# Optimization experiments

Measured on AMD Instinct MI355X. Metric: run time of the kernel, lower is better.

Reference implementation:

```python
import jax, jax.numpy as jnp
import numpy as np

N = 50000       # num_nodes
R = 32          # num_relations
H = 16          # hidden channels
C = 8           # num_classes
E = 1_600_000   # num_edges (avg degree 32)


def setup_inputs() -> dict:
    key = jax.random.key(0)
    ks = jax.random.split(key, 8)
    edge_index = jax.random.randint(ks[0], (2, E), 0, N, dtype=jnp.int64)
    edge_type = jnp.sort(jax.random.randint(ks[1], (E,), 0, R, dtype=jnp.int64))
    s1 = 1.0 / np.sqrt(N)
    s2 = 1.0 / np.sqrt(H)
    return {
        "edge_index": edge_index,
        "edge_type": edge_type,
        "weight1": jax.random.normal(ks[2], (R, N, H), jnp.float32) * s1,
        "root1": jax.random.normal(ks[3], (N, H), jnp.float32) * s1,
        "bias1": jnp.zeros((H,), jnp.float32),
        "weight2": jax.random.normal(ks[4], (R, H, C), jnp.float32) * s2,
        "root2": jax.random.normal(ks[5], (H, C), jnp.float32) * s2,
        "bias2": jnp.zeros((C,), jnp.float32),
    }


def reference(edge_index, edge_type, weight1, root1, bias1, weight2, root2, bias2):
    # R-GCN with mean aggregation per relation (PyG RGCNConv semantics).
    src, dst = edge_index[0], edge_index[1]
    # combined segment id: one segment per (relation, dst node)
    seg = edge_type * N + dst  # [E]
    ones = jnp.ones((E,), weight1.dtype)
    cnt = jax.ops.segment_sum(ones, seg, num_segments=R * N)          # [R*N]
    denom = jnp.maximum(cnt, 1.0)[:, None]

    # ---- layer 1: x = None -> identity features; message_r(j) = weight1[r, j] ----
    msg1 = weight1[edge_type, src]                                     # [E, H] gather
    mean1 = jax.ops.segment_sum(msg1, seg, num_segments=R * N) / denom # [R*N, H]
    h = mean1.reshape(R, N, H).sum(0) + root1 + bias1                  # [N, H]
    h = jax.nn.relu(h)

    # ---- layer 2: aggregate features per relation, then relation-specific GEMM ----
    msg2 = h[src]                                                       # [E, H]
    mean2 = jax.ops.segment_sum(msg2, seg, num_segments=R * N) / denom  # [R*N, H]
    mean2 = mean2.reshape(R, N, H)
    out = jnp.einsum('rnf,rfo->no', mean2, weight2) + h @ root2 + bias2 # [N, C]
    return jax.nn.log_softmax(out, axis=1)
```

## Files before the change

kernel.cpp:

```cpp
#include <hip/hip_runtime.h>
#include <math.h>

#define NN 50000
#define RR 32
#define HH 16
#define CC 8
#define SHIFT 6
#define BSZ 64
#define NB 782
#define CAP 2560
#define G 256
#define BINS (BSZ * RR)
#define SCH 64

static __device__ __forceinline__ unsigned short f2bf(float x) {
    unsigned u = __float_as_uint(x);
    unsigned r = (u + 0x7FFF + ((u >> 16) & 1)) >> 16;
    return (unsigned short)r;
}


__global__ void hist_k(const int* __restrict__ dst, int* __restrict__ hist, int E) {
    __shared__ int lh[NB];
    int g = blockIdx.x, tid = threadIdx.x;
    for (int j = tid; j < NB; j += 256) lh[j] = 0;
    __syncthreads();
    int chunk = (E + G - 1) / G;
    int beg = g * chunk, end = min(beg + chunk, E);
    for (int i = beg + tid; i < end; i += 256)
        atomicAdd(&lh[dst[i] >> SHIFT], 1);
    __syncthreads();
    for (int j = tid; j < NB; j += 256) hist[g * NB + j] = lh[j];
}

__global__ void scanAC_k(const int* __restrict__ hist, int* __restrict__ pos,
                         int* __restrict__ btot) {
    __shared__ int lds[G];
    int b = blockIdx.x, t = threadIdx.x;
    int v = hist[t * NB + b];
    lds[t] = v;
    __syncthreads();
    for (int ofs = 1; ofs < G; ofs <<= 1) {
        int add = (t >= ofs) ? lds[t - ofs] : 0;
        __syncthreads();
        lds[t] += add;
        __syncthreads();
    }
    pos[t * NB + b] = b * CAP + lds[t] - v;
    if (t == G - 1) btot[b] = lds[t];
}

__global__ void scatter2_k(const int* __restrict__ src, const int* __restrict__ dst,
                           const int* __restrict__ et, const int* __restrict__ pos,
                           unsigned* __restrict__ bucket, int E) {
    __shared__ int cur[NB];
    int g = blockIdx.x, tid = threadIdx.x;
    for (int j = tid; j < NB; j += 256) cur[j] = pos[g * NB + j];
    __syncthreads();
    int chunk = (E + G - 1) / G;
    int beg = g * chunk, end = min(beg + chunk, E);
    for (int i = beg + tid; i < end; i += 256) {
        int d = dst[i];
        int p = atomicAdd(&cur[d >> SHIFT], 1);
        bucket[p] = (unsigned)src[i] | ((unsigned)et[i] << 16) |
                    ((unsigned)(d & (BSZ - 1)) << 21);
    }
}


__global__ __launch_bounds__(256) void sortfin_k(
        const unsigned* __restrict__ bucket, const int* __restrict__ btot,
        unsigned* __restrict__ sorted, int* __restrict__ off2,
        float* __restrict__ inv) {
    __shared__ int bins[BINS];
    __shared__ unsigned stage[CAP];
    __shared__ int ts[256];
    int b = blockIdx.x, t = threadIdx.x;
    int e0 = b * CAP, n = btot[b];
    int d0 = b * BSZ;
    int ndst = NN - d0; if (ndst > BSZ) ndst = BSZ;
    for (int j = t; j < BINS; j += 256) bins[j] = 0;
    __syncthreads();
    for (int i = t; i < n; i += 256) {
        unsigned rec = bucket[e0 + i];
        int key = ((rec >> 21) & 63) * RR + ((rec >> 16) & 31);
        atomicAdd(&bins[key], 1);
    }
    __syncthreads();
    for (int j = t; j < ndst * RR; j += 256)
        inv[d0 * RR + j] = 1.0f / fmaxf((float)bins[j], 1.0f);
    int loc[8]; int s = 0;
#pragma unroll
    for (int k = 0; k < 8; ++k) { loc[k] = bins[t * 8 + k]; s += loc[k]; }
    ts[t] = s;
    __syncthreads();
    for (int ofs = 1; ofs < 256; ofs <<= 1) {
        int add = (t >= ofs) ? ts[t - ofs] : 0;
        __syncthreads();
        ts[t] += add;
        __syncthreads();
    }
    int run = ts[t] - s;
    __syncthreads();
#pragma unroll
    for (int k = 0; k < 8; ++k) { int c = loc[k]; bins[t * 8 + k] = run; run += c; }
    __syncthreads();
    for (int dl = t; dl < BSZ; dl += 256) off2[b * 65 + dl] = e0 + bins[dl * RR];
    if (t == 0) off2[b * 65 + 64] = e0 + n;
    __syncthreads();
    for (int i = t; i < n; i += 256) {
        unsigned rec = bucket[e0 + i];
        int key = ((rec >> 21) & 63) * RR + ((rec >> 16) & 31);
        int p = atomicAdd(&bins[key], 1);
        stage[p] = rec & 0x1FFFFF;
    }
    __syncthreads();
    for (int i = t; i < n; i += 256) sorted[e0 + i] = stage[i];
}


__global__ __launch_bounds__(256) void layer1_k(
        const unsigned* __restrict__ sorted, const int* __restrict__ off2,
        const float* __restrict__ inv, const float4* __restrict__ w1v,
        const float4* __restrict__ root1v, const float4* __restrict__ bias1v,
        float4* __restrict__ hv) {
    int d = (blockIdx.x * blockDim.x + threadIdx.x) >> 6;
    if (d >= NN) return;
    int lane = threadIdx.x & 63;
    int q = lane & 3, eo = lane >> 2;
    int idx = (d >> 6) * 65 + (d & 63);
    int b0 = off2[idx], b1 = off2[idx + 1];
    const float* invd = inv + d * RR;

    unsigned rec[4]; float sc[4];
#pragma unroll
    for (int k = 0; k < 4; ++k) {
        int i = b0 + eo + k * 16;
        bool ok = i < b1;
        rec[k] = ok ? sorted[i] : 0u;
        sc[k]  = ok ? invd[(rec[k] >> 16) & 31] : 0.f;
    }
    float4 w[4];
#pragma unroll
    for (int k = 0; k < 4; ++k)
        w[k] = w1v[(size_t)(((rec[k] >> 16) & 31) * NN + (rec[k] & 0xFFFF)) * 4 + q];
    float ax = 0.f, ay = 0.f, az = 0.f, aw = 0.f;
#pragma unroll
    for (int k = 0; k < 4; ++k) {
        ax += w[k].x * sc[k]; ay += w[k].y * sc[k];
        az += w[k].z * sc[k]; aw += w[k].w * sc[k];
    }
    for (int i = b0 + 64 + eo; i < b1; i += 16) {
        unsigned rr = sorted[i];
        float s2 = invd[(rr >> 16) & 31];
        float4 ww = w1v[(size_t)(((rr >> 16) & 31) * NN + (rr & 0xFFFF)) * 4 + q];
        ax += ww.x * s2; ay += ww.y * s2; az += ww.z * s2; aw += ww.w * s2;
    }
#pragma unroll
    for (int m = 4; m < 64; m <<= 1) {
        ax += __shfl_xor(ax, m); ay += __shfl_xor(ay, m);
        az += __shfl_xor(az, m); aw += __shfl_xor(aw, m);
    }
    if (lane < 4) {
        float4 rt = root1v[d * 4 + lane];
        float4 bs = bias1v[lane];
        float4 o;
        o.x = fmaxf(ax + rt.x + bs.x, 0.f);
        o.y = fmaxf(ay + rt.y + bs.y, 0.f);
        o.z = fmaxf(az + rt.z + bs.z, 0.f);
        o.w = fmaxf(aw + rt.w + bs.w, 0.f);
        hv[d * 4 + lane] = o;
    }
}


__global__ __launch_bounds__(256) void hwbuild_k(
        const float* __restrict__ h, const float* __restrict__ w2,
        unsigned* __restrict__ hw2u) {
    __shared__ float4 hs[SCH * 4];
    int tid = threadIdx.x;
    int nl = tid >> 7;
    int k  = tid & 127;
    int r  = k >> 2;
    int c0 = (k & 3) * 2;
    float wa[HH], wb[HH];
    {
        const float* base = w2 + r * HH * CC;
#pragma unroll
        for (int f = 0; f < HH; ++f) {
            wa[f] = base[f * CC + c0];
            wb[f] = base[f * CC + c0 + 1];
        }
    }
    int s0 = blockIdx.x * SCH;
    int nnodes = NN - s0; if (nnodes > SCH) nnodes = SCH;
    const float4* hg = (const float4*)(h + s0 * HH);
    for (int j = tid; j < nnodes * 4; j += 256) hs[j] = hg[j];
    __syncthreads();
    for (int sl = nl; sl < nnodes; sl += 2) {
        float4 h0 = hs[sl * 4 + 0], h1 = hs[sl * 4 + 1];
        float4 h2 = hs[sl * 4 + 2], h3 = hs[sl * 4 + 3];
        float hr[HH] = {h0.x, h0.y, h0.z, h0.w, h1.x, h1.y, h1.z, h1.w,
                        h2.x, h2.y, h2.z, h2.w, h3.x, h3.y, h3.z, h3.w};
        float va = 0.f, vb = 0.f;
#pragma unroll
        for (int f = 0; f < HH; ++f) { va += hr[f] * wa[f]; vb += hr[f] * wb[f]; }
        unsigned packed = (unsigned)f2bf(va) | ((unsigned)f2bf(vb) << 16);
        hw2u[(size_t)(s0 + sl) * 128 + k] = packed;
    }
}


__global__ __launch_bounds__(256) void layer2_k(
        const unsigned* __restrict__ sorted, const int* __restrict__ off2,
        const float* __restrict__ inv, const unsigned* __restrict__ hw2u,
        const float* __restrict__ h, const float* __restrict__ root2,
        const float* __restrict__ bias2, float* __restrict__ out) {
    int d = (blockIdx.x * blockDim.x + threadIdx.x) >> 6;
    if (d >= NN) return;
    int lane = threadIdx.x & 63;
    int sub = lane >> 2, cp = lane & 3;
    int idx = (d >> 6) * 65 + (d & 63);
    int b0 = off2[idx], b1 = off2[idx + 1];
    const float* invd = inv + d * RR;

    unsigned rec[4]; float sc[4];
#pragma unroll
    for (int k = 0; k < 4; ++k) {
        int i = b0 + sub + k * 16;
        bool ok = i < b1;
        rec[k] = ok ? sorted[i] : 0u;
        sc[k]  = ok ? invd[(rec[k] >> 16) & 31] : 0.f;
    }
    unsigned pk[4];
#pragma unroll
    for (int k = 0; k < 4; ++k)
        pk[k] = hw2u[(size_t)(rec[k] & 0xFFFF) * 128 + ((rec[k] >> 16) & 31) * 4 + cp];
    float alo = 0.f, ahi = 0.f;
#pragma unroll
    for (int k = 0; k < 4; ++k) {
        alo += __uint_as_float(pk[k] << 16) * sc[k];
        ahi += __uint_as_float(pk[k] & 0xFFFF0000u) * sc[k];
    }
    for (int i = b0 + 64 + sub; i < b1; i += 16) {
        unsigned rr = sorted[i];
        float s2 = invd[(rr >> 16) & 31];
        unsigned pp = hw2u[(size_t)(rr & 0xFFFF) * 128 + ((rr >> 16) & 31) * 4 + cp];
        alo += __uint_as_float(pp << 16) * s2;
        ahi += __uint_as_float(pp & 0xFFFF0000u) * s2;
    }
#pragma unroll
    for (int m = 4; m < 64; m <<= 1) {
        alo += __shfl_xor(alo, m);
        ahi += __shfl_xor(ahi, m);
    }
    if (lane < 4) {
        int c0 = cp * 2;
        float vlo = alo + bias2[c0];
        float vhi = ahi + bias2[c0 + 1];
        const float* hd = h + d * HH;
#pragma unroll
        for (int f = 0; f < HH; ++f) {
            float hf = hd[f];
            vlo += hf * root2[f * CC + c0];
            vhi += hf * root2[f * CC + c0 + 1];
        }
        float m = fmaxf(vlo, vhi);
        m = fmaxf(m, __shfl_xor(m, 1));
        m = fmaxf(m, __shfl_xor(m, 2));
        float ss = expf(vlo - m) + expf(vhi - m);
        ss += __shfl_xor(ss, 1);
        ss += __shfl_xor(ss, 2);
        float z = m + logf(ss);
        float2 o = make_float2(vlo - z, vhi - z);
        *(float2*)(out + d * CC + c0) = o;
    }
}


extern "C" void kernel_launch(void* const* d_in, const int* in_sizes, int n_in,
                              void* d_out, int out_size, void* d_ws, size_t ws_size,
                              hipStream_t stream) {
    const int*   edge_index = (const int*)d_in[0];
    const int*   edge_type  = (const int*)d_in[1];
    const float* weight1    = (const float*)d_in[2];
    const float* root1      = (const float*)d_in[3];
    const float* bias1      = (const float*)d_in[4];
    const float* weight2    = (const float*)d_in[5];
    const float* root2      = (const float*)d_in[6];
    const float* bias2      = (const float*)d_in[7];
    float* out = (float*)d_out;

    const int E = in_sizes[1];
    const int* src = edge_index;
    const int* dst = edge_index + E;

    char* base = (char*)d_ws;
    size_t hw2_bytes = sizeof(unsigned short) * (size_t)NN * RR * CC;
    unsigned* hw2u = (unsigned*)base;

    char* p = base;
    auto suballoc = [&](size_t bytes) -> void* {
        void* r = (void*)p; p += (bytes + 255) & ~(size_t)255; return r;
    };
    int*      hist   = (int*)     suballoc(sizeof(int) * (size_t)G * NB);
    int*      pos    = (int*)     suballoc(sizeof(int) * (size_t)G * NB);
    unsigned* bucket = (unsigned*)suballoc(sizeof(unsigned) * (size_t)NB * CAP);

    p = base + ((hw2_bytes + 255) & ~(size_t)255);
    int*      btot   = (int*)     suballoc(sizeof(int) * NB);
    int*      off2   = (int*)     suballoc(sizeof(int) * (size_t)NB * 65);
    unsigned* sorted = (unsigned*)suballoc(sizeof(unsigned) * (size_t)NB * CAP);
    float*    inv    = (float*)   suballoc(sizeof(float) * (size_t)NN * RR);
    float*    h      = (float*)   suballoc(sizeof(float) * (size_t)NN * HH);
    (void)ws_size;

    hist_k<<<G, 256, 0, stream>>>(dst, hist, E);
    scanAC_k<<<NB, G, 0, stream>>>(hist, pos, btot);
    scatter2_k<<<G, 256, 0, stream>>>(src, dst, edge_type, pos, bucket, E);
    sortfin_k<<<NB, 256, 0, stream>>>(bucket, btot, sorted, off2, inv);

    int nblk = (NN * 64 + 255) / 256;
    layer1_k<<<nblk, 256, 0, stream>>>(sorted, off2, inv, (const float4*)weight1,
                                       (const float4*)root1, (const float4*)bias1,
                                       (float4*)h);
    hwbuild_k<<<(NN + SCH - 1) / SCH, 256, 0, stream>>>(h, weight2, hw2u);
    layer2_k<<<nblk, 256, 0, stream>>>(sorted, off2, inv, hw2u, h,
                                       root2, bias2, out);
}
```

Before: 148.3 us.

## Fuse edge bucketing and sorting stages into one cooperative kernel with grid syncs

Merges the histogram, scan, scatter and per-bucket sort kernels into a single cooperative launch of 256 blocks separated by grid-wide syncs. This removes three kernel launch boundaries. The column scan is now done serially by one thread per bucket over 256 entries instead of a parallel block scan. The per-bucket sort now runs on only 256 blocks looping over 782 buckets instead of 782 independent blocks, which reduces parallelism and adds grid-sync overhead.

```diff
diff --git a/kernel.cpp b/kernel.cpp
--- a/kernel.cpp
+++ b/kernel.cpp
@@ -1,5 +1,8 @@
 #include <hip/hip_runtime.h>
+#include <hip/hip_cooperative_groups.h>
 #include <math.h>
+
+namespace cg = cooperative_groups;
 
 #define NN 50000
 #define RR 32
@@ -20,102 +23,95 @@
 }
 
 
-__global__ void hist_k(const int* __restrict__ dst, int* __restrict__ hist, int E) {
-    __shared__ int lh[NB];
-    int g = blockIdx.x, tid = threadIdx.x;
-    for (int j = tid; j < NB; j += 256) lh[j] = 0;
-    __syncthreads();
+__global__ __launch_bounds__(256) void build_k(
+        const int* __restrict__ src, const int* __restrict__ dst,
+        const int* __restrict__ et, int* __restrict__ hist, int* __restrict__ pos,
+        int* __restrict__ btot, unsigned* __restrict__ bucket,
+        unsigned* __restrict__ sorted, int* __restrict__ off2,
+        float* __restrict__ inv, int E) {
+    __shared__ int smem[BINS];
+    __shared__ unsigned stage[CAP];
+    __shared__ int ts[256];
+    cg::grid_group grid = cg::this_grid();
+    int g = blockIdx.x, t = threadIdx.x;
     int chunk = (E + G - 1) / G;
     int beg = g * chunk, end = min(beg + chunk, E);
-    for (int i = beg + tid; i < end; i += 256)
-        atomicAdd(&lh[dst[i] >> SHIFT], 1);
+
+    for (int j = t; j < NB; j += 256) smem[j] = 0;
     __syncthreads();
-    for (int j = tid; j < NB; j += 256) hist[g * NB + j] = lh[j];
-}
-
-__global__ void scanAC_k(const int* __restrict__ hist, int* __restrict__ pos,
-                         int* __restrict__ btot) {
-    __shared__ int lds[G];
-    int b = blockIdx.x, t = threadIdx.x;
-    int v = hist[t * NB + b];
-    lds[t] = v;
+    for (int i = beg + t; i < end; i += 256)
+        atomicAdd(&smem[dst[i] >> SHIFT], 1);
     __syncthreads();
-    for (int ofs = 1; ofs < G; ofs <<= 1) {
-        int add = (t >= ofs) ? lds[t - ofs] : 0;
-        __syncthreads();
-        lds[t] += add;
-        __syncthreads();
-    }
-    pos[t * NB + b] = b * CAP + lds[t] - v;
-    if (t == G - 1) btot[b] = lds[t];
-}
-
-__global__ void scatter2_k(const int* __restrict__ src, const int* __restrict__ dst,
-                           const int* __restrict__ et, const int* __restrict__ pos,
-                           unsigned* __restrict__ bucket, int E) {
-    __shared__ int cur[NB];
-    int g = blockIdx.x, tid = threadIdx.x;
-    for (int j = tid; j < NB; j += 256) cur[j] = pos[g * NB + j];
+    for (int j = t; j < NB; j += 256) hist[g * NB + j] = smem[j];
+    __threadfence();
+    grid.sync();
+
+    int T = g * 256 + t;
+    if (T < NB) {
+        int run = T * CAP;
+        for (int gg = 0; gg < G; ++gg) {
+            pos[gg * NB + T] = run;
+            run += hist[gg * NB + T];
+        }
+        btot[T] = run - T * CAP;
+    }
+    __threadfence();
+    grid.sync();
+
+    for (int j = t; j < NB; j += 256) smem[j] = pos[g * NB + j];
     __syncthreads();
-    int chunk = (E + G - 1) / G;
-    int beg = g * chunk, end = min(beg + chunk, E);
-    for (int i = beg + tid; i < end; i += 256) {
+    for (int i = beg + t; i < end; i += 256) {
         int d = dst[i];
-        int p = atomicAdd(&cur[d >> SHIFT], 1);
+        int p = atomicAdd(&smem[d >> SHIFT], 1);
         bucket[p] = (unsigned)src[i] | ((unsigned)et[i] << 16) |
                     ((unsigned)(d & (BSZ - 1)) << 21);
     }
-}
-
-
-__global__ __launch_bounds__(256) void sortfin_k(
-        const unsigned* __restrict__ bucket, const int* __restrict__ btot,
-        unsigned* __restrict__ sorted, int* __restrict__ off2,
-        float* __restrict__ inv) {
-    __shared__ int bins[BINS];
-    __shared__ unsigned stage[CAP];
-    __shared__ int ts[256];
-    int b = blockIdx.x, t = threadIdx.x;
-    int e0 = b * CAP, n = btot[b];
-    int d0 = b * BSZ;
-    int ndst = NN - d0; if (ndst > BSZ) ndst = BSZ;
-    for (int j = t; j < BINS; j += 256) bins[j] = 0;
-    __syncthreads();
-    for (int i = t; i < n; i += 256) {
-        unsigned rec = bucket[e0 + i];
-        int key = ((rec >> 21) & 63) * RR + ((rec >> 16) & 31);
-        atomicAdd(&bins[key], 1);
-    }
-    __syncthreads();
-    for (int j = t; j < ndst * RR; j += 256)
-        inv[d0 * RR + j] = 1.0f / fmaxf((float)bins[j], 1.0f);
-    int loc[8]; int s = 0;
-#pragma unroll
-    for (int k = 0; k < 8; ++k) { loc[k] = bins[t * 8 + k]; s += loc[k]; }
-    ts[t] = s;
-    __syncthreads();
-    for (int ofs = 1; ofs < 256; ofs <<= 1) {
-        int add = (t >= ofs) ? ts[t - ofs] : 0;
-        __syncthreads();
-        ts[t] += add;
-        __syncthreads();
-    }
-    int run = ts[t] - s;
-    __syncthreads();
-#pragma unroll
-    for (int k = 0; k < 8; ++k) { int c = loc[k]; bins[t * 8 + k] = run; run += c; }
-    __syncthreads();
-    for (int dl = t; dl < BSZ; dl += 256) off2[b * 65 + dl] = e0 + bins[dl * RR];
-    if (t == 0) off2[b * 65 + 64] = e0 + n;
-    __syncthreads();
-    for (int i = t; i < n; i += 256) {
-        unsigned rec = bucket[e0 + i];
-        int key = ((rec >> 21) & 63) * RR + ((rec >> 16) & 31);
-        int p = atomicAdd(&bins[key], 1);
-        stage[p] = rec & 0x1FFFFF;
-    }
-    __syncthreads();
-    for (int i = t; i < n; i += 256) sorted[e0 + i] = stage[i];
+    __threadfence();
+    grid.sync();
+
+    for (int b = g; b < NB; b += G) {
+        int e0 = b * CAP, n = btot[b];
+        int d0 = b * BSZ;
+        int ndst = NN - d0; if (ndst > BSZ) ndst = BSZ;
+        __syncthreads();
+        for (int j = t; j < BINS; j += 256) smem[j] = 0;
+        __syncthreads();
+        for (int i = t; i < n; i += 256) {
+            unsigned rec = bucket[e0 + i];
+            int key = ((rec >> 21) & 63) * RR + ((rec >> 16) & 31);
+            atomicAdd(&smem[key], 1);
+        }
+        __syncthreads();
+        for (int j = t; j < ndst * RR; j += 256)
+            inv[d0 * RR + j] = 1.0f / fmaxf((float)smem[j], 1.0f);
+        int loc[8]; int s = 0;
+#pragma unroll
+        for (int k = 0; k < 8; ++k) { loc[k] = smem[t * 8 + k]; s += loc[k]; }
+        ts[t] = s;
+        __syncthreads();
+        for (int ofs = 1; ofs < 256; ofs <<= 1) {
+            int add = (t >= ofs) ? ts[t - ofs] : 0;
+            __syncthreads();
+            ts[t] += add;
+            __syncthreads();
+        }
+        int run = ts[t] - s;
+        __syncthreads();
+#pragma unroll
+        for (int k = 0; k < 8; ++k) { int c = loc[k]; smem[t * 8 + k] = run; run += c; }
+        __syncthreads();
+        for (int dl = t; dl < BSZ; dl += 256) off2[b * 65 + dl] = e0 + smem[dl * RR];
+        if (t == 0) off2[b * 65 + 64] = e0 + n;
+        __syncthreads();
+        for (int i = t; i < n; i += 256) {
+            unsigned rec = bucket[e0 + i];
+            int key = ((rec >> 21) & 63) * RR + ((rec >> 16) & 31);
+            int p = atomicAdd(&smem[key], 1);
+            stage[p] = rec & 0x1FFFFF;
+        }
+        __syncthreads();
+        for (int i = t; i < n; i += 256) sorted[e0 + i] = stage[i];
+    }
 }
 
 
@@ -315,10 +311,12 @@
     float*    h      = (float*)   suballoc(sizeof(float) * (size_t)NN * HH);
     (void)ws_size;
 
-    hist_k<<<G, 256, 0, stream>>>(dst, hist, E);
-    scanAC_k<<<NB, G, 0, stream>>>(hist, pos, btot);
-    scatter2_k<<<G, 256, 0, stream>>>(src, dst, edge_type, pos, bucket, E);
-    sortfin_k<<<NB, 256, 0, stream>>>(bucket, btot, sorted, off2, inv);
+    int E_ = E;
+    void* args[] = {(void*)&src, (void*)&dst, (void*)&edge_type,
+                    (void*)&hist, (void*)&pos, (void*)&btot,
+                    (void*)&bucket, (void*)&sorted, (void*)&off2,
+                    (void*)&inv, (void*)&E_};
+    hipLaunchCooperativeKernel((void*)build_k, dim3(G), dim3(256), args, 0, stream);
 
     int nblk = (NN * 64 + 255) / 256;
     layer1_k<<<nblk, 256, 0, stream>>>(sorted, off2, inv, (const float4*)weight1,
```

Measured after the change: 336.2 us. +126.7%, slower.
